# Kernel tuning notes

Hardware: AMD Instinct MI355X
Metric: run time of the kernel (lower is better)

## Reference

```python
import jax, jax.numpy as jnp
import numpy as np
from itertools import combinations

B = 512
N_FEATURES = 64
BINS = 64
N_EMBED = 32
N_HIDDEN = 128
N_OUTPUT = 1
GAMMA = 1.0
TOTAL = N_FEATURES * BINS  # sum(feature_sizes) = 4096


def setup_inputs() -> dict:
    key = jax.random.key(0)
    ks = jax.random.split(key, 20)
    P = N_FEATURES * (N_FEATURES - 1) // 2  # 2016
    mains = jax.random.randint(ks[0], (B, N_FEATURES), 0, BINS, dtype=jnp.int32)
    pairs = jax.random.randint(ks[1], (B, P, 2), 0, BINS, dtype=jnp.int32)
    emb = jax.random.normal(ks[2], (TOTAL, N_EMBED), dtype=jnp.float32) * 0.05
    s = 0.05
    mw0 = jax.random.normal(ks[3], (N_FEATURES, N_EMBED, N_HIDDEN), jnp.float32) * s
    mw1 = jax.random.normal(ks[4], (N_FEATURES, N_HIDDEN, N_HIDDEN), jnp.float32) * s
    mw2 = jax.random.normal(ks[5], (N_FEATURES, N_HIDDEN, N_OUTPUT), jnp.float32) * s
    mb0 = jax.random.normal(ks[6], (N_FEATURES, N_HIDDEN), jnp.float32) * s
    mb1 = jax.random.normal(ks[7], (N_FEATURES, N_HIDDEN), jnp.float32) * s
    mb2 = jax.random.normal(ks[8], (N_FEATURES, N_OUTPUT), jnp.float32) * s
    z_main = jax.random.uniform(ks[9], (N_FEATURES,), jnp.float32, -GAMMA / 100, GAMMA / 100)
    pw0 = jax.random.normal(ks[10], (P, 2 * N_EMBED, N_HIDDEN), jnp.float32) * s
    pw1 = jax.random.normal(ks[11], (P, N_HIDDEN, N_HIDDEN), jnp.float32) * s
    pw2 = jax.random.normal(ks[12], (P, N_HIDDEN, N_OUTPUT), jnp.float32) * s
    pb0 = jax.random.normal(ks[13], (P, N_HIDDEN), jnp.float32) * s
    pb1 = jax.random.normal(ks[14], (P, N_HIDDEN), jnp.float32) * s
    pb2 = jax.random.normal(ks[15], (P, N_OUTPUT), jnp.float32) * s
    z_pairs = jax.random.uniform(ks[16], (P,), jnp.float32, -GAMMA / 100, GAMMA / 100)
    pairs_list = jnp.asarray(np.array(list(combinations(range(N_FEATURES), 2)), dtype=np.int32))
    feature_offsets = (jnp.arange(N_FEATURES, dtype=jnp.int32) * BINS)
    return dict(mains=mains, pairs=pairs, emb=emb,
                mw0=mw0, mw1=mw1, mw2=mw2, mb0=mb0, mb1=mb1, mb2=mb2, z_main=z_main,
                pw0=pw0, pw1=pw1, pw2=pw2, pb0=pb0, pb1=pb1, pb2=pb2, z_pairs=z_pairs,
                pairs_list=pairs_list, feature_offsets=feature_offsets)


def _smooth_z(z):
    g = GAMMA
    smooth = (-2.0 / g ** 3) * z ** 3 + (3.0 / (2.0 * g)) * z + 0.5
    return jnp.where(z <= -g / 2, 0.0, jnp.where(z >= g / 2, 1.0, smooth))


def _grouped_mlp(h, ws, bs):
    # h: [B, G, d_in]; ws[i]: [G, d_in_i, d_out_i]; relu on all but last layer
    n = len(ws)
    for i, (w, b) in enumerate(zip(ws, bs)):
        h = jnp.einsum('bgk,gkl->bgl', h, w) + b[None]
        if i < n - 1:
            h = jax.nn.relu(h)
    return h


def reference(mains, pairs, emb, mw0, mw1, mw2, mb0, mb1, mb2, z_main,
              pw0, pw1, pw2, pb0, pb1, pb2, z_pairs, pairs_list, feature_offsets):
    # main effects: per-feature embedding gather + per-feature MLP
    main_idx = mains + feature_offsets[None, :]             # [B, F]
    h = emb[main_idx]                                        # [B, F, E]
    h = _grouped_mlp(h, [mw0, mw1, mw2], [mb0, mb1, mb2])    # [B, F, O]
    zm = _smooth_z(z_main)                                   # [F]
    out_main = jnp.einsum('bfo,f->bo', h, zm)                # [B, O]
    # pair effects: gather both feature embeddings, concat, per-pair MLP
    pair_off = feature_offsets[pairs_list]                   # [P, 2]
    pair_idx = pairs + pair_off[None]                        # [B, P, 2]
    e = emb[pair_idx]                                        # [B, P, 2, E]
    Bp, P = e.shape[0], e.shape[1]
    e = e.reshape(Bp, P, 2 * e.shape[-1])                    # [B, P, 2E]
    hp = _grouped_mlp(e, [pw0, pw1, pw2], [pb0, pb1, pb2])   # [B, P, O]
    zp = _smooth_z(z_pairs)                                  # [P]
    out_pairs = jnp.einsum('bpo,p->bo', hp, zp)              # [B, O]
    return out_main + out_pairs
```

## Files before the change

### kernel.cpp

```cpp
#include <hip/hip_runtime.h>


typedef _Float16 f16x8 __attribute__((ext_vector_type(8)));
typedef _Float16 f16x4 __attribute__((ext_vector_type(4)));
typedef float f32x4 __attribute__((ext_vector_type(4)));

constexpr int Bsz = 512;
constexpr int NF  = 64;
constexpr int NE  = 32;
constexpr int NH  = 128;
constexpr int NP  = 2016;
constexpr int NG  = NP + NF;
constexpr int BT  = 64;
constexpr int NSEG = 8, GSEG = NG / NSEG;

constexpr size_t WS_S2 = (size_t)NG * Bsz;
constexpr size_t WS_PT = WS_S2 + (size_t)NSEG * Bsz;

__device__ __forceinline__ float smoothz(float z) {
  float s = fmaf(-2.0f * z * z, z, fmaf(1.5f, z, 0.5f));
  if (z <= -0.5f) s = 0.0f;
  if (z >=  0.5f) s = 1.0f;
  return s;
}

__global__ void transpose_pairs_kernel(const int* __restrict__ pairs,
                                       int* __restrict__ pt) {
  __shared__ int tile[32][33];
  const int bt = blockIdx.x;
  const int qt = blockIdx.y;
  const int t  = threadIdx.x;
  const int tq = t & 7, tb = t >> 3;
  const int brow  = bt * 32 + tb;
  const int qbase = qt * 32 + tq * 4;
#pragma unroll
  for (int j = 0; j < 4; ++j)
    tile[tb][tq * 4 + j] = pairs[brow * (2 * NP) + qbase + j];
  __syncthreads();
  const int ob = t & 7, oq = t >> 3;
  const int qrow = qt * 32 + oq;
#pragma unroll
  for (int j = 0; j < 4; ++j)
    pt[(size_t)qrow * Bsz + bt * 32 + ob * 4 + j] = tile[ob * 4 + j][oq];
}

__device__ __forceinline__ f16x8 load_col_frag(const float* __restrict__ p) {
  f16x8 f;
#pragma unroll
  for (int j = 0; j < 8; ++j) f[j] = (_Float16)p[(size_t)(j * NH)];
  return f;
}

__global__ __launch_bounds__(256, 3) void fused_groups_kernel(
    const int* __restrict__ mains, const int* __restrict__ pt,
    const float* __restrict__ emb,
    const float* __restrict__ mw0, const float* __restrict__ mw1,
    const float* __restrict__ mw2, const float* __restrict__ mb0,
    const float* __restrict__ mb1, const float* __restrict__ mb2,
    const float* __restrict__ z_main,
    const float* __restrict__ pw0, const float* __restrict__ pw1,
    const float* __restrict__ pw2, const float* __restrict__ pb0,
    const float* __restrict__ pb1, const float* __restrict__ pb2,
    const float* __restrict__ z_pairs,
    const int* __restrict__ pairs_list, const int* __restrict__ foff,
    float* __restrict__ ws) {
  __shared__ _Float16 sA[BT * 64];
  __shared__ _Float16 sH[BT * NH];
  __shared__ __align__(16) float sBias[3 * NH];
  __shared__ float sRed[4 * BT];

  const int t    = threadIdx.x;
  const int wave = t >> 6;
  const int lane = t & 63;
  const int l    = lane & 15;
  const int qd   = lane >> 4;
  const int g    = blockIdx.x;
  const bool is_pair = (g < NP);

  const float *W0, *W1, *w2p, *bv0, *bv1;
  float b2s, z;
  int off0 = 0, off1 = 0, fid = 0;
  if (is_pair) {
    W0  = pw0 + (size_t)g * (2 * NE * NH);
    W1  = pw1 + (size_t)g * (NH * NH);
    w2p = pw2 + (size_t)g * NH;
    bv0 = pb0 + (size_t)g * NH;
    bv1 = pb1 + (size_t)g * NH;
    b2s = pb2[g];
    z   = smoothz(z_pairs[g]);
    off0 = foff[pairs_list[2 * g + 0]];
    off1 = foff[pairs_list[2 * g + 1]];
  } else {
    fid = g - NP;
    W0  = mw0 + (size_t)fid * (NE * NH);
    W1  = mw1 + (size_t)fid * (NH * NH);
    w2p = mw2 + (size_t)fid * NH;
    bv0 = mb0 + (size_t)fid * NH;
    bv1 = mb1 + (size_t)fid * NH;
    b2s = mb2[fid];
    z   = smoothz(z_main[fid]);
    off0 = foff[fid];
  }

  if (t < 96) {
    const int which = t >> 5;
    const int i = (t & 31) * 4;
    const float* src = which == 0 ? bv0 : (which == 1 ? bv1 : w2p);
    *(float4*)&sBias[which * NH + i] = *(const float4*)(src + i);
  }

  const int hq = wave * 32 + l;
  f16x8 w0f[2][2];
  f16x8 w1f[2][4];
#pragma unroll
  for (int mh = 0; mh < 2; ++mh) {
    const float* base0 = W0 + (size_t)(qd * 8) * NH + (hq + mh * 16);
    w0f[mh][0] = load_col_frag(base0);
    if (is_pair) w0f[mh][1] = load_col_frag(base0 + (size_t)32 * NH);
  }
#pragma unroll
  for (int mh = 0; mh < 2; ++mh)
#pragma unroll
    for (int kb = 0; kb < 4; ++kb)
      w1f[mh][kb] =
          load_col_frag(W1 + (size_t)(kb * 32 + qd * 8) * NH + (hq + mh * 16));

  const int hq4 = wave * 32 + qd * 4;

  for (int tile = 0; tile < Bsz / BT; ++tile) {
    const int bbase = tile * BT;

    {
      const int row = t & 63;
      const int q   = t >> 6;
      const int b   = bbase + row;
      if (is_pair) {
        const int which = q >> 1;
        const int bin = pt[(size_t)(2 * g + which) * Bsz + b];
        const int idx = bin + (which ? off1 : off0);
        const float* er = emb + (size_t)idx * NE + (q & 1) * 16;
        const float4 e0 = ((const float4*)er)[0];
        const float4 e1 = ((const float4*)er)[1];
        const float4 e2 = ((const float4*)er)[2];
        const float4 e3 = ((const float4*)er)[3];
        f16x8 h0, h1;
        h0[0] = (_Float16)e0.x; h0[1] = (_Float16)e0.y;
        h0[2] = (_Float16)e0.z; h0[3] = (_Float16)e0.w;
        h0[4] = (_Float16)e1.x; h0[5] = (_Float16)e1.y;
        h0[6] = (_Float16)e1.z; h0[7] = (_Float16)e1.w;
        h1[0] = (_Float16)e2.x; h1[1] = (_Float16)e2.y;
        h1[2] = (_Float16)e2.z; h1[3] = (_Float16)e2.w;
        h1[4] = (_Float16)e3.x; h1[5] = (_Float16)e3.y;
        h1[6] = (_Float16)e3.z; h1[7] = (_Float16)e3.w;
        const int blk0 = (2 * q)     ^ (row & 7);
        const int blk1 = (2 * q + 1) ^ (row & 7);
        *(f16x8*)&sA[row * 64 + blk0 * 8] = h0;
        *(f16x8*)&sA[row * 64 + blk1 * 8] = h1;
      } else {
        const int bin = mains[b * NF + fid];
        const int idx = bin + off0;
        const float* er = emb + (size_t)idx * NE + q * 8;
        const float4 e0 = ((const float4*)er)[0];
        const float4 e1 = ((const float4*)er)[1];
        f16x8 h0;
        h0[0] = (_Float16)e0.x; h0[1] = (_Float16)e0.y;
        h0[2] = (_Float16)e0.z; h0[3] = (_Float16)e0.w;
        h0[4] = (_Float16)e1.x; h0[5] = (_Float16)e1.y;
        h0[6] = (_Float16)e1.z; h0[7] = (_Float16)e1.w;
        const int blk = q ^ (row & 7);
        *(f16x8*)&sA[row * 64 + blk * 8] = h0;
      }
    }
    __syncthreads();

    f32x4 acc0[2][4];
#pragma unroll
    for (int mh = 0; mh < 2; ++mh) {
      const f32x4 b0q = *(const f32x4*)&sBias[hq4 + mh * 16];
#pragma unroll
      for (int nb = 0; nb < 4; ++nb) acc0[mh][nb] = b0q;
    }
#pragma unroll
    for (int nb = 0; nb < 4; ++nb) {
      const int b  = nb * 16 + l;
      const int rs = b & 7;
      const f16x8 e0 = *(const f16x8*)&sA[b * 64 + ((qd ^ rs) * 8)];
      acc0[0][nb] = __builtin_amdgcn_mfma_f32_16x16x32_f16(w0f[0][0], e0,
                                                           acc0[0][nb], 0, 0, 0);
      acc0[1][nb] = __builtin_amdgcn_mfma_f32_16x16x32_f16(w0f[1][0], e0,
                                                           acc0[1][nb], 0, 0, 0);
      if (is_pair) {
        const f16x8 e1 = *(const f16x8*)&sA[b * 64 + (((4 + qd) ^ rs) * 8)];
        acc0[0][nb] = __builtin_amdgcn_mfma_f32_16x16x32_f16(w0f[0][1], e1,
                                                             acc0[0][nb], 0, 0, 0);
        acc0[1][nb] = __builtin_amdgcn_mfma_f32_16x16x32_f16(w0f[1][1], e1,
                                                             acc0[1][nb], 0, 0, 0);
      }
    }

#pragma unroll
    for (int mh = 0; mh < 2; ++mh) {
      const int hb = hq4 + mh * 16;
#pragma unroll
      for (int nb = 0; nb < 4; ++nb) {
        const int b = nb * 16 + l;
        f16x4 h4;
#pragma unroll
        for (int r = 0; r < 4; ++r)
          h4[r] = (_Float16)fmaxf(acc0[mh][nb][r], 0.0f);
        const int blk = (hb >> 3) ^ (b & 7);
        *(f16x4*)&sH[b * NH + blk * 8 + (hb & 7)] = h4;
      }
    }
    __syncthreads();

    f32x4 acc1[2][4];
#pragma unroll
    for (int mh = 0; mh < 2; ++mh) {
      const f32x4 b1q = *(const f32x4*)&sBias[NH + hq4 + mh * 16];
#pragma unroll
      for (int nb = 0; nb < 4; ++nb) acc1[mh][nb] = b1q;
    }
#pragma unroll
    for (int kb = 0; kb < 4; ++kb) {
#pragma unroll
      for (int nb = 0; nb < 4; ++nb) {
        const int b = nb * 16 + l;
        const f16x8 hf =
            *(const f16x8*)&sH[b * NH + (((kb * 4 + qd) ^ (b & 7)) * 8)];
        acc1[0][nb] = __builtin_amdgcn_mfma_f32_16x16x32_f16(w1f[0][kb], hf,
                                                             acc1[0][nb], 0, 0, 0);
        acc1[1][nb] = __builtin_amdgcn_mfma_f32_16x16x32_f16(w1f[1][kb], hf,
                                                             acc1[1][nb], 0, 0, 0);
      }
    }

    float yp[4] = {0.0f, 0.0f, 0.0f, 0.0f};
#pragma unroll
    for (int mh = 0; mh < 2; ++mh) {
      const f32x4 w2q = *(const f32x4*)&sBias[2 * NH + hq4 + mh * 16];
#pragma unroll
      for (int nb = 0; nb < 4; ++nb)
#pragma unroll
        for (int r = 0; r < 4; ++r)
          yp[nb] = fmaf(fmaxf(acc1[mh][nb][r], 0.0f), w2q[r], yp[nb]);
    }
#pragma unroll
    for (int nb = 0; nb < 4; ++nb) {
      yp[nb] += __shfl_xor(yp[nb], 16, 64);
      yp[nb] += __shfl_xor(yp[nb], 32, 64);
    }
    if (qd == 0) {
#pragma unroll
      for (int nb = 0; nb < 4; ++nb) sRed[wave * BT + nb * 16 + l] = yp[nb];
    }
    __syncthreads();
    if (t < BT) {
      const float s =
          sRed[t] + sRed[BT + t] + sRed[2 * BT + t] + sRed[3 * BT + t];
      ws[(size_t)g * Bsz + bbase + t] = (s + b2s) * z;
    }
  }
}

__global__ void reduce1_kernel(const float* __restrict__ part,
                               float* __restrict__ s2) {
  const int b   = blockIdx.x * 256 + threadIdx.x;
  const int seg = blockIdx.y;
  float s = 0.0f;
#pragma unroll 8
  for (int g = seg * GSEG; g < (seg + 1) * GSEG; ++g)
    s += part[(size_t)g * Bsz + b];
  s2[seg * Bsz + b] = s;
}

__global__ void reduce2_kernel(const float* __restrict__ s2,
                               float* __restrict__ out) {
  const int b = blockIdx.x * 256 + threadIdx.x;
  float s = 0.0f;
#pragma unroll
  for (int k = 0; k < NSEG; ++k) s += s2[k * Bsz + b];
  out[b] = s;
}

extern "C" void kernel_launch(void* const* d_in, const int* in_sizes, int n_in,
                              void* d_out, int out_size, void* d_ws,
                              size_t ws_size, hipStream_t stream) {
  const int*   mains      = (const int*)d_in[0];
  const int*   pairs      = (const int*)d_in[1];
  const float* emb        = (const float*)d_in[2];
  const float* mw0        = (const float*)d_in[3];
  const float* mw1        = (const float*)d_in[4];
  const float* mw2        = (const float*)d_in[5];
  const float* mb0        = (const float*)d_in[6];
  const float* mb1        = (const float*)d_in[7];
  const float* mb2        = (const float*)d_in[8];
  const float* z_main     = (const float*)d_in[9];
  const float* pw0        = (const float*)d_in[10];
  const float* pw1        = (const float*)d_in[11];
  const float* pw2        = (const float*)d_in[12];
  const float* pb0        = (const float*)d_in[13];
  const float* pb1        = (const float*)d_in[14];
  const float* pb2        = (const float*)d_in[15];
  const float* z_pairs    = (const float*)d_in[16];
  const int*   pairs_list = (const int*)d_in[17];
  const int*   foff       = (const int*)d_in[18];
  float* ws   = (float*)d_ws;
  float* out  = (float*)d_out;
  float* part = ws;
  float* s2   = ws + WS_S2;
  int*   pt   = (int*)(ws + WS_PT);

  transpose_pairs_kernel<<<dim3(16, 126), 256, 0, stream>>>(pairs, pt);
  fused_groups_kernel<<<NG, 256, 0, stream>>>(
      mains, pt, emb, mw0, mw1, mw2, mb0, mb1, mb2, z_main, pw0, pw1, pw2,
      pb0, pb1, pb2, z_pairs, pairs_list, foff, part);
  reduce1_kernel<<<dim3(2, NSEG), 256, 0, stream>>>(part, s2);
  reduce2_kernel<<<2, 256, 0, stream>>>(s2, out);
}
```

Measured before the change: 339.5 us.

## Double-buffer embedding tiles and prefetch bin indices to overlap gathers with MFMA

Preloads all per-tile bin indices into registers up front and double-buffers the shared embedding tile, so the next tile's global embedding gather is issued before the current tile's MFMA work and written to the other buffer afterwards. The weight fragment loads are moved ahead of the bias staging, and launch bounds are raised to ask for four blocks per SM. This is meant to hide gather latency behind compute. The costs are extra registers for the prefetched indices and in-flight embedding values, possible spills under the tighter occupancy bound, and twice the shared memory for the input tile.

```diff
diff --git a/kernel.cpp b/kernel.cpp
--- a/kernel.cpp
+++ b/kernel.cpp
@@ -12,6 +12,7 @@
 constexpr int NP  = 2016;
 constexpr int NG  = NP + NF;
 constexpr int BT  = 64;
+constexpr int NT  = Bsz / BT;
 constexpr int NSEG = 8, GSEG = NG / NSEG;
 
 constexpr size_t WS_S2 = (size_t)NG * Bsz;
@@ -51,7 +52,7 @@
   return f;
 }
 
-__global__ __launch_bounds__(256, 3) void fused_groups_kernel(
+__global__ __launch_bounds__(256, 4) void fused_groups_kernel(
     const int* __restrict__ mains, const int* __restrict__ pt,
     const float* __restrict__ emb,
     const float* __restrict__ mw0, const float* __restrict__ mw1,
@@ -64,7 +65,7 @@
     const float* __restrict__ z_pairs,
     const int* __restrict__ pairs_list, const int* __restrict__ foff,
     float* __restrict__ ws) {
-  __shared__ _Float16 sA[BT * 64];
+  __shared__ _Float16 sA[2][BT * 64];
   __shared__ _Float16 sH[BT * NH];
   __shared__ __align__(16) float sBias[3 * NH];
   __shared__ float sRed[4 * BT];
@@ -102,6 +103,22 @@
     off0 = foff[fid];
   }
 
+  const int hq = wave * 32 + l;
+  f16x8 w0f[2][2];
+  f16x8 w1f[2][4];
+#pragma unroll
+  for (int mh = 0; mh < 2; ++mh) {
+    const float* base0 = W0 + (size_t)(qd * 8) * NH + (hq + mh * 16);
+    w0f[mh][0] = load_col_frag(base0);
+    if (is_pair) w0f[mh][1] = load_col_frag(base0 + (size_t)32 * NH);
+  }
+#pragma unroll
+  for (int mh = 0; mh < 2; ++mh)
+#pragma unroll
+    for (int kb = 0; kb < 4; ++kb)
+      w1f[mh][kb] =
+          load_col_frag(W1 + (size_t)(kb * 32 + qd * 8) * NH + (hq + mh * 16));
+
   if (t < 96) {
     const int which = t >> 5;
     const int i = (t & 31) * 4;
@@ -109,69 +126,70 @@
     *(float4*)&sBias[which * NH + i] = *(const float4*)(src + i);
   }
 
-  const int hq = wave * 32 + l;
-  f16x8 w0f[2][2];
-  f16x8 w1f[2][4];
-#pragma unroll
-  for (int mh = 0; mh < 2; ++mh) {
-    const float* base0 = W0 + (size_t)(qd * 8) * NH + (hq + mh * 16);
-    w0f[mh][0] = load_col_frag(base0);
-    if (is_pair) w0f[mh][1] = load_col_frag(base0 + (size_t)32 * NH);
-  }
-#pragma unroll
-  for (int mh = 0; mh < 2; ++mh)
-#pragma unroll
-    for (int kb = 0; kb < 4; ++kb)
-      w1f[mh][kb] =
-          load_col_frag(W1 + (size_t)(kb * 32 + qd * 8) * NH + (hq + mh * 16));
+  const int row = t & 63;
+  const int q   = t >> 6;
+  const int myoff = is_pair ? ((q >> 1) ? off1 : off0) : off0;
+  int binv[NT];
+  if (is_pair) {
+    const size_t pbase = (size_t)(2 * g + (q >> 1)) * Bsz + row;
+#pragma unroll
+    for (int i = 0; i < NT; ++i) binv[i] = pt[pbase + i * BT];
+  } else {
+#pragma unroll
+    for (int i = 0; i < NT; ++i) binv[i] = mains[(i * BT + row) * NF + fid];
+  }
+
+  float4 er0, er1, er2, er3;
+  auto ldemb = [&](int tl) {
+    const int idx = binv[tl] + myoff;
+    const float* er =
+        emb + (size_t)idx * NE + (is_pair ? ((q & 1) * 16) : (q * 8));
+    er0 = ((const float4*)er)[0];
+    er1 = ((const float4*)er)[1];
+    if (is_pair) {
+      er2 = ((const float4*)er)[2];
+      er3 = ((const float4*)er)[3];
+    }
+  };
+  auto stemb = [&](int buf) {
+    if (is_pair) {
+      f16x8 h0, h1;
+      h0[0] = (_Float16)er0.x; h0[1] = (_Float16)er0.y;
+      h0[2] = (_Float16)er0.z; h0[3] = (_Float16)er0.w;
+      h0[4] = (_Float16)er1.x; h0[5] = (_Float16)er1.y;
+      h0[6] = (_Float16)er1.z; h0[7] = (_Float16)er1.w;
+      h1[0] = (_Float16)er2.x; h1[1] = (_Float16)er2.y;
+      h1[2] = (_Float16)er2.z; h1[3] = (_Float16)er2.w;
+      h1[4] = (_Float16)er3.x; h1[5] = (_Float16)er3.y;
+      h1[6] = (_Float16)er3.z; h1[7] = (_Float16)er3.w;
+      const int blk0 = (2 * q)     ^ (row & 7);
+      const int blk1 = (2 * q + 1) ^ (row & 7);
+      *(f16x8*)&sA[buf][row * 64 + blk0 * 8] = h0;
+      *(f16x8*)&sA[buf][row * 64 + blk1 * 8] = h1;
+    } else {
+      f16x8 h0;
+      h0[0] = (_Float16)er0.x; h0[1] = (_Float16)er0.y;
+      h0[2] = (_Float16)er0.z; h0[3] = (_Float16)er0.w;
+      h0[4] = (_Float16)er1.x; h0[5] = (_Float16)er1.y;
+      h0[6] = (_Float16)er1.z; h0[7] = (_Float16)er1.w;
+      const int blk = q ^ (row & 7);
+      *(f16x8*)&sA[buf][row * 64 + blk * 8] = h0;
+    }
+  };
+
+  ldemb(0);
+  stemb(0);
+  __syncthreads();
 
   const int hq4 = wave * 32 + qd * 4;
 
-  for (int tile = 0; tile < Bsz / BT; ++tile) {
+#pragma unroll
+  for (int tile = 0; tile < NT; ++tile) {
+    const int c = tile & 1;
+    const _Float16* sAc = sA[c];
     const int bbase = tile * BT;
 
-    {
-      const int row = t & 63;
-      const int q   = t >> 6;
-      const int b   = bbase + row;
-      if (is_pair) {
-        const int which = q >> 1;
-        const int bin = pt[(size_t)(2 * g + which) * Bsz + b];
-        const int idx = bin + (which ? off1 : off0);
-        const float* er = emb + (size_t)idx * NE + (q & 1) * 16;
-        const float4 e0 = ((const float4*)er)[0];
-        const float4 e1 = ((const float4*)er)[1];
-        const float4 e2 = ((const float4*)er)[2];
-        const float4 e3 = ((const float4*)er)[3];
-        f16x8 h0, h1;
-        h0[0] = (_Float16)e0.x; h0[1] = (_Float16)e0.y;
-        h0[2] = (_Float16)e0.z; h0[3] = (_Float16)e0.w;
-        h0[4] = (_Float16)e1.x; h0[5] = (_Float16)e1.y;
-        h0[6] = (_Float16)e1.z; h0[7] = (_Float16)e1.w;
-        h1[0] = (_Float16)e2.x; h1[1] = (_Float16)e2.y;
-        h1[2] = (_Float16)e2.z; h1[3] = (_Float16)e2.w;
-        h1[4] = (_Float16)e3.x; h1[5] = (_Float16)e3.y;
-        h1[6] = (_Float16)e3.z; h1[7] = (_Float16)e3.w;
-        const int blk0 = (2 * q)     ^ (row & 7);
-        const int blk1 = (2 * q + 1) ^ (row & 7);
-        *(f16x8*)&sA[row * 64 + blk0 * 8] = h0;
-        *(f16x8*)&sA[row * 64 + blk1 * 8] = h1;
-      } else {
-        const int bin = mains[b * NF + fid];
-        const int idx = bin + off0;
-        const float* er = emb + (size_t)idx * NE + q * 8;
-        const float4 e0 = ((const float4*)er)[0];
-        const float4 e1 = ((const float4*)er)[1];
-        f16x8 h0;
-        h0[0] = (_Float16)e0.x; h0[1] = (_Float16)e0.y;
-        h0[2] = (_Float16)e0.z; h0[3] = (_Float16)e0.w;
-        h0[4] = (_Float16)e1.x; h0[5] = (_Float16)e1.y;
-        h0[6] = (_Float16)e1.z; h0[7] = (_Float16)e1.w;
-        const int blk = q ^ (row & 7);
-        *(f16x8*)&sA[row * 64 + blk * 8] = h0;
-      }
-    }
-    __syncthreads();
+    if (tile + 1 < NT) ldemb(tile + 1);
 
     f32x4 acc0[2][4];
 #pragma unroll
@@ -184,13 +202,13 @@
     for (int nb = 0; nb < 4; ++nb) {
       const int b  = nb * 16 + l;
       const int rs = b & 7;
-      const f16x8 e0 = *(const f16x8*)&sA[b * 64 + ((qd ^ rs) * 8)];
+      const f16x8 e0 = *(const f16x8*)&sAc[b * 64 + ((qd ^ rs) * 8)];
       acc0[0][nb] = __builtin_amdgcn_mfma_f32_16x16x32_f16(w0f[0][0], e0,
                                                            acc0[0][nb], 0, 0, 0);
       acc0[1][nb] = __builtin_amdgcn_mfma_f32_16x16x32_f16(w0f[1][0], e0,
                                                            acc0[1][nb], 0, 0, 0);
       if (is_pair) {
-        const f16x8 e1 = *(const f16x8*)&sA[b * 64 + (((4 + qd) ^ rs) * 8)];
+        const f16x8 e1 = *(const f16x8*)&sAc[b * 64 + (((4 + qd) ^ rs) * 8)];
         acc0[0][nb] = __builtin_amdgcn_mfma_f32_16x16x32_f16(w0f[0][1], e1,
                                                              acc0[0][nb], 0, 0, 0);
         acc0[1][nb] = __builtin_amdgcn_mfma_f32_16x16x32_f16(w0f[1][1], e1,
@@ -254,6 +272,9 @@
 #pragma unroll
       for (int nb = 0; nb < 4; ++nb) sRed[wave * BT + nb * 16 + l] = yp[nb];
     }
+
+    if (tile + 1 < NT) stemb(c ^ 1);
+
     __syncthreads();
     if (t < BT) {
       const float s =
```

After: 391.7 us. 1.15x slower.
